# Optimization experiments

Measured on AMD Instinct MI355X. Metric: run time of the kernel, lower is better.

Reference implementation:

```python
import jax, jax.numpy as jnp
import numpy as np

N, E, G = 30000, 240000, 128
D_IN, D_H, D_OUT, HEADS = 128, 128, 16, 4
EPS_BN = 1e-5


def setup_inputs() -> dict:
    key = jax.random.key(0)
    ks = jax.random.split(key, 24)
    s = 0.1
    inp = {
        "x": jax.random.normal(ks[0], (N, D_IN), jnp.float32),
        "edge_index": jax.random.randint(ks[1], (2, E), 0, N, jnp.int32),
        "batch": jnp.sort(jax.random.randint(ks[2], (N,), 0, G, jnp.int32)),
        # stacked per-layer params (3 GAT blocks, identical shapes since D_IN==D_H)
        "W": jax.random.normal(ks[3], (3, D_H, HEADS * D_H), jnp.float32) * s,
        "att_src": jax.random.normal(ks[4], (3, HEADS, D_H), jnp.float32) * s,
        "att_dst": jax.random.normal(ks[5], (3, HEADS, D_H), jnp.float32) * s,
        "conv_b": jnp.zeros((3, D_H), jnp.float32),
        "gamma": jnp.ones((3, D_H), jnp.float32),
        "beta": jnp.zeros((3, D_H), jnp.float32),
        "sk_Win": jax.random.normal(ks[6], (3, D_H, D_H), jnp.float32) * s,
        "sk_bin": jnp.zeros((3, D_H), jnp.float32),
        "sk_Wout": jax.random.normal(ks[7], (3, D_H, D_H), jnp.float32) * s,
        "sk_bout": jnp.zeros((3, D_H), jnp.float32),
        "fc1_W": jax.random.normal(ks[8], (D_H, D_H), jnp.float32) * s,
        "fc1_b": jnp.zeros((D_H,), jnp.float32),
        "fc3_W": jax.random.normal(ks[9], (D_H, D_OUT), jnp.float32) * s,
        "fc3_b": jnp.zeros((D_OUT,), jnp.float32),
    }
    return inp


def _gat_conv(x, src, dst, W, a_src, a_dst, b):
    # PyG GATConv, heads=4, concat=False (mean over heads), leaky_relu 0.2
    h = (x @ W).reshape(N, HEADS, D_H)                      # [N,H,C]
    al_s = jnp.einsum('nhc,hc->nh', h, a_src)               # [N,H]
    al_d = jnp.einsum('nhc,hc->nh', h, a_dst)
    e = jax.nn.leaky_relu(al_s[src] + al_d[dst], 0.2)       # [Etot,H]
    m = jax.ops.segment_max(e, dst, num_segments=N)
    m = jnp.where(jnp.isfinite(m), m, 0.0)
    ex = jnp.exp(e - m[dst])
    z = jax.ops.segment_sum(ex, dst, num_segments=N)
    alpha = ex / (z[dst] + 1e-16)                           # [Etot,H]
    msg = h[src] * alpha[:, :, None]                        # [Etot,H,C]
    out = jax.ops.segment_sum(msg, dst, num_segments=N)     # [N,H,C]
    return out.mean(axis=1) + b


def _batch_norm(h, gamma, beta):
    mu = h.mean(axis=0)
    var = h.var(axis=0)
    return gamma * (h - mu) * jax.lax.rsqrt(var + EPS_BN) + beta


def _gated_skip(in_x, out_x, Win, bin_, Wout, bout):
    gate = jax.nn.sigmoid(in_x @ Win + bin_ + out_x @ Wout + bout)
    return gate * out_x + (1.0 - gate) * in_x


def reference(x, edge_index, batch, W, att_src, att_dst, conv_b, gamma, beta,
              sk_Win, sk_bin, sk_Wout, sk_bout, fc1_W, fc1_b, fc3_W, fc3_b):
    # add self loops (PyG GATConv default)
    loops = jnp.arange(N, dtype=edge_index.dtype)
    src = jnp.concatenate([edge_index[0], loops])
    dst = jnp.concatenate([edge_index[1], loops])

    h = x
    for l in range(3):
        idn = h
        h = _gat_conv(h, src, dst, W[l], att_src[l], att_dst[l], conv_b[l])
        h = _batch_norm(h, gamma[l], beta[l])
        h = _gated_skip(idn, h, sk_Win[l], sk_bin[l], sk_Wout[l], sk_bout[l])
        h = jax.nn.relu(h)

    # global mean pool over graphs
    cnt = jax.ops.segment_sum(jnp.ones((N,), h.dtype), batch, num_segments=G)
    hg = jax.ops.segment_sum(h, batch, num_segments=G) / jnp.maximum(cnt, 1.0)[:, None]
    hg = jax.nn.relu(hg @ fc1_W + fc1_b)
    return hg @ fc3_W + fc3_b
```

## Files before the change

kernel.cpp:

```cpp
#include <hip/hip_runtime.h>
#include <hip/hip_bf16.h>

#define N_NODES 30000
#define N_EDGES 240000
#define ETOT    (N_EDGES + N_NODES)
#define NGRAPH  128
#define NBLK    118
#define NWAVES  4096

typedef __attribute__((ext_vector_type(8))) short bf16x8;
typedef __attribute__((ext_vector_type(4))) short bf16x4;
typedef __attribute__((ext_vector_type(4))) float f32x4;

__device__ __forceinline__ unsigned short f2bf(float f) {
    unsigned u = __float_as_uint(f);
    u += 0x7fff + ((u >> 16) & 1);
    return (unsigned short)(u >> 16);
}
__device__ __forceinline__ float bf2f(unsigned short h) {
    return __uint_as_float(((unsigned)h) << 16);
}

__global__ __launch_bounds__(256) void prep_kernel(const float* __restrict__ W,
                                                   const float* __restrict__ Win,
                                                   const float* __restrict__ Wout,
                                                   const float* __restrict__ x,
                                                   const int* __restrict__ batch,
                                                   short* __restrict__ wt_hi,
                                                   short* __restrict__ wint_hi,
                                                   short* __restrict__ woutt_hi,
                                                   short* __restrict__ xb,
                                                   int* __restrict__ gstart,
                                                   int* __restrict__ deg,
                                                   float* __restrict__ bnsum) {
    int i = blockIdx.x * 256 + threadIdx.x;
    if (i < 196608) {
        int l = i >> 16, r = i & 65535;
        int n = r >> 7, k = r & 127;
        wt_hi[i] = (short)f2bf(W[(size_t)l * 65536 + k * 512 + n]);
    } else if (i < 245760) {
        int j = i - 196608;
        int l = j >> 14, r = j & 16383;
        int n = r >> 7, k = r & 127;
        wint_hi[j] = (short)f2bf(Win[(size_t)l * 16384 + k * 128 + n]);
    } else if (i < 294912) {
        int j = i - 245760;
        int l = j >> 14, r = j & 16383;
        int n = r >> 7, k = r & 127;
        woutt_hi[j] = (short)f2bf(Wout[(size_t)l * 16384 + k * 128 + n]);
    } else if (i < 774912) {
        int j = i - 294912;
        const float4* p = (const float4*)x + (size_t)j * 2;
        float4 v0 = p[0], v1 = p[1];
        bf16x8 hv;
        hv[0] = (short)f2bf(v0.x); hv[1] = (short)f2bf(v0.y);
        hv[2] = (short)f2bf(v0.z); hv[3] = (short)f2bf(v0.w);
        hv[4] = (short)f2bf(v1.x); hv[5] = (short)f2bf(v1.y);
        hv[6] = (short)f2bf(v1.z); hv[7] = (short)f2bf(v1.w);
        *(bf16x8*)(xb + (size_t)j * 8) = hv;
    } else if (i < 775041) {
        int t = i - 774912;
        int lo = 0, hi = N_NODES;
        while (lo < hi) { int mid = (lo + hi) >> 1; if (batch[mid] < t) lo = mid + 1; else hi = mid; }
        gstart[t] = lo;
    } else if (i < 805041) {
        deg[i - 775041] = 0;
    } else if (i < 805809) {
        bnsum[i - 805041] = 0.f;
    }
}

__global__ __launch_bounds__(256) void gemm_conv(const short* __restrict__ Ab,
                                                 const short* __restrict__ Bth,
                                                 const float* __restrict__ att_s,
                                                 const float* __restrict__ att_d,
                                                 unsigned short* __restrict__ hfullb,
                                                 float* __restrict__ als,
                                                 float* __restrict__ ald) {
    __shared__ short As_h[64 * 136];
    __shared__ float red_s[2][64], red_d[2][64];
    const int bm = blockIdx.x * 64;
    const int hd = blockIdx.y;
    const int bn = hd * 128;
    const int t  = threadIdx.x;
#pragma unroll
    for (int i = 0; i < 4; i++) {
        int idx8 = t + i * 256;
        int row = idx8 >> 4, c8 = (idx8 & 15) << 3;
        bf16x8 vh = {};
        if (bm + row < N_NODES)
            vh = *(const bf16x8*)(Ab + (size_t)(bm + row) * 128 + c8);
        *(bf16x8*)(As_h + row * 136 + c8) = vh;
    }
    __syncthreads();

    const int w = t >> 6, lane = t & 63;
    const int wr = w >> 1, wc = w & 1;
    const int lr = lane & 15, lg = lane >> 4;
    f32x4 acc[2][4] = {};
    const size_t bofs0 = (size_t)(bn + wc * 64 + lr) * 128 + lg * 8;
#pragma unroll
    for (int kk = 0; kk < 4; kk++) {
        bf16x8 ah[2], bh[4];
#pragma unroll
        for (int ni = 0; ni < 4; ni++) {
            size_t o = bofs0 + (size_t)ni * 16 * 128 + kk * 32;
            bh[ni] = *(const bf16x8*)(Bth + o);
        }
        int ko = kk * 32 + lg * 8;
#pragma unroll
        for (int mi = 0; mi < 2; mi++) {
            int r = wr * 32 + mi * 16 + lr;
            ah[mi] = *(const bf16x8*)(As_h + r * 136 + ko);
        }
#pragma unroll
        for (int mi = 0; mi < 2; mi++)
#pragma unroll
            for (int ni = 0; ni < 4; ni++)
                acc[mi][ni] = __builtin_amdgcn_mfma_f32_16x16x32_bf16(ah[mi], bh[ni], acc[mi][ni], 0, 0, 0);
    }
    float as_c[4], ad_c[4];
#pragma unroll
    for (int ni = 0; ni < 4; ni++) {
        int cc = wc * 64 + ni * 16 + lr;
        as_c[ni] = att_s[hd * 128 + cc];
        ad_c[ni] = att_d[hd * 128 + cc];
    }
#pragma unroll
    for (int mi = 0; mi < 2; mi++) {
#pragma unroll
        for (int r = 0; r < 4; r++) {
            float ps = 0.f, pd = 0.f;
#pragma unroll
            for (int ni = 0; ni < 4; ni++) {
                ps = fmaf(acc[mi][ni][r], as_c[ni], ps);
                pd = fmaf(acc[mi][ni][r], ad_c[ni], pd);
            }
#pragma unroll
            for (int off = 1; off < 16; off <<= 1) {
                ps += __shfl_xor(ps, off);
                pd += __shfl_xor(pd, off);
            }
            if (lr == 0) {
                int row = wr * 32 + mi * 16 + lg * 4 + r;
                red_s[wc][row] = ps;
                red_d[wc][row] = pd;
            }
        }
    }
    __syncthreads();
#pragma unroll
    for (int mi = 0; mi < 2; mi++)
#pragma unroll
        for (int ni = 0; ni < 4; ni++) {
            int nl = wc * 64 + ni * 16 + lr;
#pragma unroll
            for (int r = 0; r < 4; r++) {
                int row = wr * 32 + mi * 16 + lg * 4 + r;
                As_h[row * 136 + nl] = (short)f2bf(acc[mi][ni][r]);
            }
        }
    if (t < 64) {
        int m = bm + t;
        if (m < N_NODES) als[m * 4 + hd] = red_s[0][t] + red_s[1][t];
    } else if (t < 128) {
        int tt = t - 64;
        int m = bm + tt;
        if (m < N_NODES) ald[m * 4 + hd] = red_d[0][tt] + red_d[1][tt];
    }
    __syncthreads();
#pragma unroll
    for (int i2 = 0; i2 < 4; i2++) {
        int idx8 = t + i2 * 256;
        int row = idx8 >> 4, c8 = (idx8 & 15) << 3;
        int m = bm + row;
        if (m < N_NODES)
            *(bf16x8*)(hfullb + (size_t)m * 512 + bn + c8) = *(const bf16x8*)(As_h + row * 136 + c8);
    }
}

__global__ __launch_bounds__(256) void skip_conv(const short* __restrict__ hinb,
                                                 const float* __restrict__ g,
                                                 const float* __restrict__ bnsum,
                                                 const float* __restrict__ gamma,
                                                 const float* __restrict__ beta,
                                                 const short* __restrict__ w1h,
                                                 const short* __restrict__ w2h,
                                                 const float* __restrict__ bin,
                                                 const float* __restrict__ bout,
                                                 const short* __restrict__ wtn,
                                                 const float* __restrict__ att_s,
                                                 const float* __restrict__ att_d,
                                                 short* __restrict__ houtb,
                                                 unsigned short* __restrict__ hfullb,
                                                 float* __restrict__ als,
                                                 float* __restrict__ ald) {
    __shared__ short A1h[64 * 136], A2h[64 * 136];
    __shared__ float bnp_s[256];
    __shared__ float redS[4][64], redD[4][64];
    const int bm = blockIdx.x * 64;
    const int t  = threadIdx.x;
    if (t < 128) {
        float inv = 1.f / (float)N_NODES;
        float mu  = bnsum[t] * inv;
        float var = bnsum[128 + t] * inv - mu * mu;
        float rs  = rsqrtf(var + 1e-5f);
        float sc  = gamma[t] * rs;
        bnp_s[t]       = sc;
        bnp_s[128 + t] = beta[t] - mu * sc;
    }
    __syncthreads();
#pragma unroll
    for (int i = 0; i < 4; i++) {
        int idx8 = t + i * 256;
        int row = idx8 >> 4, c8 = (idx8 & 15) << 3;
        bf16x8 vh = {};
        if (bm + row < N_NODES)
            vh = *(const bf16x8*)(hinb + (size_t)(bm + row) * 128 + c8);
        *(bf16x8*)(A1h + row * 136 + c8) = vh;
    }
#pragma unroll
    for (int i = 0; i < 8; i++) {
        int idx4 = t + i * 256;
        int row = idx4 >> 5, c4 = (idx4 & 31) << 2;
        float4 v2 = make_float4(0.f, 0.f, 0.f, 0.f);
        if (bm + row < N_NODES) {
            float4 gv = *(const float4*)(g + (size_t)(bm + row) * 128 + c4);
            v2.x = fmaf(bnp_s[c4 + 0], gv.x, bnp_s[128 + c4 + 0]);
            v2.y = fmaf(bnp_s[c4 + 1], gv.y, bnp_s[128 + c4 + 1]);
            v2.z = fmaf(bnp_s[c4 + 2], gv.z, bnp_s[128 + c4 + 2]);
            v2.w = fmaf(bnp_s[c4 + 3], gv.w, bnp_s[128 + c4 + 3]);
        }
        *(bf16x4*)(A2h + row * 136 + c4) = (bf16x4){(short)f2bf(v2.x), (short)f2bf(v2.y),
                                                    (short)f2bf(v2.z), (short)f2bf(v2.w)};
    }
    __syncthreads();

    const int w = t >> 6, lane = t & 63;
    const int wr = w >> 1, wc = w & 1;
    const int lr = lane & 15, lg = lane >> 4;

    {
        f32x4 acc[2][4] = {};
        const size_t bo = (size_t)(wc * 64 + lr) * 128 + lg * 8;
#pragma unroll
        for (int kk = 0; kk < 4; kk++) {
            bf16x8 a1[2], a2[2], b1[4], b2[4];
#pragma unroll
            for (int ni = 0; ni < 4; ni++) {
                size_t o = bo + (size_t)ni * 2048 + kk * 32;
                b1[ni] = *(const bf16x8*)(w1h + o);
                b2[ni] = *(const bf16x8*)(w2h + o);
            }
            int ko = kk * 32 + lg * 8;
#pragma unroll
            for (int mi = 0; mi < 2; mi++) {
                int r = wr * 32 + mi * 16 + lr;
                a1[mi] = *(const bf16x8*)(A1h + r * 136 + ko);
                a2[mi] = *(const bf16x8*)(A2h + r * 136 + ko);
            }
#pragma unroll
            for (int mi = 0; mi < 2; mi++)
#pragma unroll
                for (int ni = 0; ni < 4; ni++) {
                    acc[mi][ni] = __builtin_amdgcn_mfma_f32_16x16x32_bf16(a1[mi], b1[ni], acc[mi][ni], 0, 0, 0);
                    acc[mi][ni] = __builtin_amdgcn_mfma_f32_16x16x32_bf16(a2[mi], b2[ni], acc[mi][ni], 0, 0, 0);
                }
        }
#pragma unroll
        for (int mi = 0; mi < 2; mi++)
#pragma unroll
            for (int ni = 0; ni < 4; ni++) {
                int n = wc * 64 + ni * 16 + lr;
                float bsum = bin[n] + bout[n];
                float sc = bnp_s[n], shb = bnp_s[128 + n];
#pragma unroll
                for (int r = 0; r < 4; r++) {
                    int lrow = wr * 32 + mi * 16 + lg * 4 + r;
                    int m = bm + lrow;
                    float gv = (m < N_NODES) ? g[(size_t)m * 128 + n] : 0.f;
                    float hbnv = fmaf(sc, gv, shb);
                    float hv   = bf2f((unsigned short)A1h[lrow * 136 + n]);
                    float gt   = 1.f / (1.f + __expf(-(acc[mi][ni][r] + bsum)));
                    acc[mi][ni][r] = fmaxf(gt * hbnv + (1.f - gt) * hv, 0.f);
                }
            }
        __syncthreads();
#pragma unroll
        for (int mi = 0; mi < 2; mi++)
#pragma unroll
            for (int ni = 0; ni < 4; ni++) {
                int n = wc * 64 + ni * 16 + lr;
#pragma unroll
                for (int r = 0; r < 4; r++) {
                    int lrow = wr * 32 + mi * 16 + lg * 4 + r;
                    A1h[lrow * 136 + n] = (short)f2bf(acc[mi][ni][r]);
                }
            }
        __syncthreads();
#pragma unroll
        for (int i2 = 0; i2 < 4; i2++) {
            int idx8 = t + i2 * 256;
            int row = idx8 >> 4, c8 = (idx8 & 15) << 3;
            int m = bm + row;
            if (m < N_NODES)
                *(bf16x8*)(houtb + (size_t)m * 128 + c8) = *(const bf16x8*)(A1h + row * 136 + c8);
        }
    }

    f32x4 c2[4][8] = {};
    const int hd = w;
    const size_t bo2 = (size_t)(hd * 128 + lr) * 128 + lg * 8;
#pragma unroll
    for (int kk = 0; kk < 4; kk++) {
        bf16x8 ah2[4], bh2[8];
#pragma unroll
        for (int ni = 0; ni < 8; ni++)
            bh2[ni] = *(const bf16x8*)(wtn + bo2 + (size_t)ni * 2048 + kk * 32);
        int ko = kk * 32 + lg * 8;
#pragma unroll
        for (int mi = 0; mi < 4; mi++)
            ah2[mi] = *(const bf16x8*)(A1h + (mi * 16 + lr) * 136 + ko);
#pragma unroll
        for (int mi = 0; mi < 4; mi++)
#pragma unroll
            for (int ni = 0; ni < 8; ni++)
                c2[mi][ni] = __builtin_amdgcn_mfma_f32_16x16x32_bf16(ah2[mi], bh2[ni], c2[mi][ni], 0, 0, 0);
    }
    {
        float asc[8], adc[8];
#pragma unroll
        for (int ni = 0; ni < 8; ni++) {
            int cc = ni * 16 + lr;
            asc[ni] = att_s[hd * 128 + cc];
            adc[ni] = att_d[hd * 128 + cc];
        }
#pragma unroll
        for (int mi = 0; mi < 4; mi++)
#pragma unroll
            for (int r = 0; r < 4; r++) {
                float ps = 0.f, pd = 0.f;
#pragma unroll
                for (int ni = 0; ni < 8; ni++) {
                    ps = fmaf(c2[mi][ni][r], asc[ni], ps);
                    pd = fmaf(c2[mi][ni][r], adc[ni], pd);
                }
#pragma unroll
                for (int off = 1; off < 16; off <<= 1) {
                    ps += __shfl_xor(ps, off);
                    pd += __shfl_xor(pd, off);
                }
                if (lr == 0) {
                    int row = mi * 16 + lg * 4 + r;
                    redS[hd][row] = ps;
                    redD[hd][row] = pd;
                }
            }
    }
    __syncthreads();
    if (w < 2) {
        short* dst = (w == 0) ? A1h : A2h;
#pragma unroll
        for (int mi = 0; mi < 4; mi++)
#pragma unroll
            for (int ni = 0; ni < 8; ni++)
#pragma unroll
                for (int r = 0; r < 4; r++)
                    dst[(mi * 16 + lg * 4 + r) * 136 + ni * 16 + lr] = (short)f2bf(c2[mi][ni][r]);
    }
    {
        int hd2 = t >> 6, row = t & 63;
        int m = bm + row;
        if (m < N_NODES) {
            als[m * 4 + hd2] = redS[hd2][row];
            ald[m * 4 + hd2] = redD[hd2][row];
        }
    }
    __syncthreads();
#pragma unroll
    for (int it = 0; it < 8; it++) {
        int idx = t + it * 256;
        int row = idx >> 5, c8 = (idx & 31) << 3;
        int m = bm + row;
        if (m < N_NODES) {
            const short* src = (c8 < 128) ? A1h : A2h;
            *(bf16x8*)(hfullb + (size_t)m * 512 + c8) = *(const bf16x8*)(src + row * 136 + (c8 & 127));
        }
    }
    __syncthreads();
    if (w >= 2) {
        short* dst = (w == 2) ? A1h : A2h;
#pragma unroll
        for (int mi = 0; mi < 4; mi++)
#pragma unroll
            for (int ni = 0; ni < 8; ni++)
#pragma unroll
                for (int r = 0; r < 4; r++)
                    dst[(mi * 16 + lg * 4 + r) * 136 + ni * 16 + lr] = (short)f2bf(c2[mi][ni][r]);
    }
    __syncthreads();
#pragma unroll
    for (int it = 0; it < 8; it++) {
        int idx = t + it * 256;
        int row = idx >> 5, c8 = (idx & 31) << 3;
        int m = bm + row;
        if (m < N_NODES) {
            const short* src = (c8 < 128) ? A1h : A2h;
            *(bf16x8*)(hfullb + (size_t)m * 512 + 256 + c8) = *(const bf16x8*)(src + row * 136 + (c8 & 127));
        }
    }
}

__global__ __launch_bounds__(256) void skip_gate(const short* __restrict__ hinb,
                                                 const float* __restrict__ g,
                                                 const float* __restrict__ bnsum,
                                                 const float* __restrict__ gamma,
                                                 const float* __restrict__ beta,
                                                 const short* __restrict__ w1h,
                                                 const short* __restrict__ w2h,
                                                 const float* __restrict__ bin, const float* __restrict__ bout,
                                                 short* __restrict__ houtb) {
    __shared__ short A1h[64 * 136], A2h[64 * 136], A2l[64 * 136];
    __shared__ float bnp_s[256];
    const int bm = blockIdx.x * 64;
    const int bn = blockIdx.y * 64;
    const int t  = threadIdx.x;
    if (t < 128) {
        float inv = 1.f / (float)N_NODES;
        float mu  = bnsum[t] * inv;
        float var = bnsum[128 + t] * inv - mu * mu;
        float rs  = rsqrtf(var + 1e-5f);
        float sc  = gamma[t] * rs;
        bnp_s[t]       = sc;
        bnp_s[128 + t] = beta[t] - mu * sc;
    }
    __syncthreads();
#pragma unroll
    for (int i = 0; i < 4; i++) {
        int idx8 = t + i * 256;
        int row = idx8 >> 4, c8 = (idx8 & 15) << 3;
        bf16x8 vh = {};
        if (bm + row < N_NODES)
            vh = *(const bf16x8*)(hinb + (size_t)(bm + row) * 128 + c8);
        *(bf16x8*)(A1h + row * 136 + c8) = vh;
    }
#pragma unroll
    for (int i = 0; i < 8; i++) {
        int idx4 = t + i * 256;
        int row = idx4 >> 5, c4 = (idx4 & 31) << 2;
        float4 v2 = make_float4(0.f, 0.f, 0.f, 0.f);
        if (bm + row < N_NODES) {
            float4 gv = *(const float4*)(g + (size_t)(bm + row) * 128 + c4);
            v2.x = fmaf(bnp_s[c4 + 0], gv.x, bnp_s[128 + c4 + 0]);
            v2.y = fmaf(bnp_s[c4 + 1], gv.y, bnp_s[128 + c4 + 1]);
            v2.z = fmaf(bnp_s[c4 + 2], gv.z, bnp_s[128 + c4 + 2]);
            v2.w = fmaf(bnp_s[c4 + 3], gv.w, bnp_s[128 + c4 + 3]);
        }
        unsigned short b0 = f2bf(v2.x), b1 = f2bf(v2.y), b2 = f2bf(v2.z), b3 = f2bf(v2.w);
        *(bf16x4*)(A2h + row * 136 + c4) = (bf16x4){(short)b0, (short)b1, (short)b2, (short)b3};
        *(bf16x4*)(A2l + row * 136 + c4) = (bf16x4){(short)f2bf(v2.x - bf2f(b0)), (short)f2bf(v2.y - bf2f(b1)),
                                                    (short)f2bf(v2.z - bf2f(b2)), (short)f2bf(v2.w - bf2f(b3))};
    }
    __syncthreads();

    const int w = t >> 6, lane = t & 63;
    const int wr = w >> 1, wc = w & 1;
    const int lr = lane & 15, lg = lane >> 4;
    f32x4 acc[2][2] = {};
    const size_t bofs0 = (size_t)(bn + wc * 32 + lr) * 128 + lg * 8;
#pragma unroll
    for (int kk = 0; kk < 4; kk++) {
        bf16x8 a1f[2], a2f[2], b1h[2], b2h[2];
#pragma unroll
        for (int ni = 0; ni < 2; ni++) {
            size_t o = bofs0 + (size_t)ni * 16 * 128 + kk * 32;
            b1h[ni] = *(const bf16x8*)(w1h + o);
            b2h[ni] = *(const bf16x8*)(w2h + o);
        }
        int ko = kk * 32 + lg * 8;
#pragma unroll
        for (int mi = 0; mi < 2; mi++) {
            int r = wr * 32 + mi * 16 + lr;
            a1f[mi] = *(const bf16x8*)(A1h + r * 136 + ko);
            a2f[mi] = *(const bf16x8*)(A2h + r * 136 + ko);
        }
#pragma unroll
        for (int mi = 0; mi < 2; mi++)
#pragma unroll
            for (int ni = 0; ni < 2; ni++) {
                acc[mi][ni] = __builtin_amdgcn_mfma_f32_16x16x32_bf16(a1f[mi], b1h[ni], acc[mi][ni], 0, 0, 0);
                acc[mi][ni] = __builtin_amdgcn_mfma_f32_16x16x32_bf16(a2f[mi], b2h[ni], acc[mi][ni], 0, 0, 0);
            }
    }
#pragma unroll
    for (int mi = 0; mi < 2; mi++) {
#pragma unroll
        for (int ni = 0; ni < 2; ni++) {
            int n = bn + wc * 32 + ni * 16 + lr;
            float bsum = bin[n] + bout[n];
#pragma unroll
            for (int r = 0; r < 4; r++) {
                int lrow = wr * 32 + mi * 16 + lg * 4 + r;
                float hbnv = bf2f((unsigned short)A2h[lrow * 136 + n]) + bf2f((unsigned short)A2l[lrow * 136 + n]);
                float hv   = bf2f((unsigned short)A1h[lrow * 136 + n]);
                float gt   = 1.f / (1.f + __expf(-(acc[mi][ni][r] + bsum)));
                acc[mi][ni][r] = fmaxf(gt * hbnv + (1.f - gt) * hv, 0.f);
            }
        }
    }
    __syncthreads();
#pragma unroll
    for (int mi = 0; mi < 2; mi++)
#pragma unroll
        for (int ni = 0; ni < 2; ni++) {
            int n = bn + wc * 32 + ni * 16 + lr;
#pragma unroll
            for (int r = 0; r < 4; r++) {
                int lrow = wr * 32 + mi * 16 + lg * 4 + r;
                A1h[lrow * 136 + n] = (short)f2bf(acc[mi][ni][r]);
            }
        }
    __syncthreads();
#pragma unroll
    for (int i2 = 0; i2 < 2; i2++) {
        int idx8 = t + i2 * 256;
        int row = idx8 >> 3, c8 = (idx8 & 7) << 3;
        int m = bm + row;
        if (m < N_NODES)
            *(bf16x8*)(houtb + (size_t)m * 128 + bn + c8) = *(const bf16x8*)(A1h + row * 136 + bn + c8);
    }
}

__global__ __launch_bounds__(256) void deg_kernel(const int* __restrict__ ei1,
                                                  int* __restrict__ deg) {
    int e = blockIdx.x * 256 + threadIdx.x;
    if (e >= ETOT) return;
    int d = (e < N_EDGES) ? ei1[e] : (e - N_EDGES);
    atomicAdd(&deg[d], 1);
}

__global__ __launch_bounds__(256) void scan1(const int* __restrict__ deg,
                                             int* __restrict__ tmp,
                                             int* __restrict__ blksum) {
    int i = blockIdx.x * 256 + threadIdx.x;
    int v = (i < N_NODES) ? deg[i] : 0;
    __shared__ int sh[256];
    sh[threadIdx.x] = v;
    __syncthreads();
    int acc = v;
    for (int off = 1; off < 256; off <<= 1) {
        int u = (threadIdx.x >= off) ? sh[threadIdx.x - off] : 0;
        __syncthreads();
        acc += u;
        sh[threadIdx.x] = acc;
        __syncthreads();
    }
    if (i < N_NODES) tmp[i] = acc - v;
    if (threadIdx.x == 255) blksum[blockIdx.x] = acc;
}

__global__ void scan2(const int* __restrict__ blksum, int* __restrict__ blkoff) {
    int t = threadIdx.x;
    int v = (t < NBLK) ? blksum[t] : 0;
    __shared__ int sh[128];
    sh[t] = v;
    __syncthreads();
    int acc = v;
    for (int off = 1; off < 128; off <<= 1) {
        int u = (t >= off) ? sh[t - off] : 0;
        __syncthreads();
        acc += u;
        sh[t] = acc;
        __syncthreads();
    }
    if (t < NBLK) blkoff[t] = acc - v;
}

__global__ __launch_bounds__(256) void scan3(const int* __restrict__ tmp,
                                             const int* __restrict__ blkoff,
                                             int* __restrict__ rowptr,
                                             int* __restrict__ wofs) {
    int i = blockIdx.x * 256 + threadIdx.x;
    if (i == 0) rowptr[N_NODES] = ETOT;
    if (i < N_NODES) {
        int r = tmp[i] + blkoff[blockIdx.x];
        rowptr[i] = r;
        wofs[i]   = r;
    }
}

__global__ __launch_bounds__(256) void wpart_kernel(const int* __restrict__ rowptr,
                                                    int* __restrict__ wstart) {
    int wid = blockIdx.x * 256 + threadIdx.x;
    if (wid > NWAVES) return;
    if (wid == NWAVES) { wstart[NWAVES] = N_NODES; return; }
    int target = (int)(((long)wid * ETOT) / NWAVES);
    int lo = 0, hi = N_NODES;
    while (lo < hi) { int mid = (lo + hi) >> 1; if (rowptr[mid] < target) lo = mid + 1; else hi = mid; }
    wstart[wid] = lo;
}

__global__ __launch_bounds__(256) void scatter_kernel(const int* __restrict__ ei0,
                                                      const int* __restrict__ ei1,
                                                      int* __restrict__ wofs,
                                                      int* __restrict__ csr_src) {
    int e = blockIdx.x * 256 + threadIdx.x;
    if (e >= ETOT) return;
    int s = (e < N_EDGES) ? ei0[e] : (e - N_EDGES);
    int d = (e < N_EDGES) ? ei1[e] : (e - N_EDGES);
    int pos = atomicAdd(&wofs[d], 1);
    csr_src[pos] = s;
}

__global__ __launch_bounds__(256) void gat_gather(const int* __restrict__ rowptr,
                                                  const int* __restrict__ wstart,
                                                  const int* __restrict__ csr_src,
                                                  const float* __restrict__ al_s,
                                                  const float* __restrict__ al_d,
                                                  const unsigned short* __restrict__ hfullb,
                                                  const float* __restrict__ conv_b,
                                                  float* __restrict__ g,
                                                  float* __restrict__ bnsum,
                                                  float* __restrict__ bnsum2) {
    const int lane = threadIdx.x & 63;
    const int wib  = threadIdx.x >> 6;
    const int gwid = blockIdx.x * 4 + wib;
    const int h    = lane >> 4;
    const int sub  = lane & 15;
    float s1[8] = {}, s2[8] = {};

    const int n0 = wstart[gwid], n1 = wstart[gwid + 1];
    for (int n = n0; n < n1; n++) {
        const int e0 = rowptr[n], e1 = rowptr[n + 1];
        const float ald_h = al_d[n * 4 + h];

        float acc[8] = {};
        float zs = 0.f;
        int i = e0;
        for (; i + 3 < e1; i += 4) {
            int sA = csr_src[i], sB = csr_src[i + 1], sC = csr_src[i + 2], sD = csr_src[i + 3];
            bf16x8 ha = *(const bf16x8*)(hfullb + (size_t)sA * 512 + lane * 8);
            bf16x8 hb = *(const bf16x8*)(hfullb + (size_t)sB * 512 + lane * 8);
            bf16x8 hc = *(const bf16x8*)(hfullb + (size_t)sC * 512 + lane * 8);
            bf16x8 hd = *(const bf16x8*)(hfullb + (size_t)sD * 512 + lane * 8);
            float vA = al_s[sA * 4 + h] + ald_h; vA = (vA > 0.f) ? vA : 0.2f * vA;
            float vB = al_s[sB * 4 + h] + ald_h; vB = (vB > 0.f) ? vB : 0.2f * vB;
            float vC = al_s[sC * 4 + h] + ald_h; vC = (vC > 0.f) ? vC : 0.2f * vC;
            float vD = al_s[sD * 4 + h] + ald_h; vD = (vD > 0.f) ? vD : 0.2f * vD;
            float exA = __expf(vA), exB = __expf(vB), exC = __expf(vC), exD = __expf(vD);
            zs += (exA + exB) + (exC + exD);
#pragma unroll
            for (int j = 0; j < 8; j++) {
                float a = fmaf(exA, bf2f((unsigned short)ha[j]), acc[j]);
                a = fmaf(exB, bf2f((unsigned short)hb[j]), a);
                a = fmaf(exC, bf2f((unsigned short)hc[j]), a);
                acc[j] = fmaf(exD, bf2f((unsigned short)hd[j]), a);
            }
        }
        for (; i < e1; i++) {
            int sA = csr_src[i];
            bf16x8 ha = *(const bf16x8*)(hfullb + (size_t)sA * 512 + lane * 8);
            float vA = al_s[sA * 4 + h] + ald_h; vA = (vA > 0.f) ? vA : 0.2f * vA;
            float exA = __expf(vA);
            zs += exA;
#pragma unroll
            for (int j = 0; j < 8; j++)
                acc[j] = fmaf(exA, bf2f((unsigned short)ha[j]), acc[j]);
        }

        float inv = 0.25f / (zs + 1e-16f);
#pragma unroll
        for (int j = 0; j < 8; j++) {
            float a = acc[j] * inv;
            a += __shfl_xor(a, 16);
            a += __shfl_xor(a, 32);
            acc[j] = a;
        }
        if (lane < 16) {
            float o[8];
#pragma unroll
            for (int j = 0; j < 8; j++) {
                float tv = acc[j] + conv_b[sub * 8 + j];
                o[j] = tv;
                s1[j] += tv;
                s2[j] = fmaf(tv, tv, s2[j]);
            }
            float* gp = g + (size_t)n * 128 + sub * 8;
            *(float4*)gp       = make_float4(o[0], o[1], o[2], o[3]);
            *(float4*)(gp + 4) = make_float4(o[4], o[5], o[6], o[7]);
        }
    }

    __shared__ float redA[4][128], redB[4][128];
    if (lane < 16) {
#pragma unroll
        for (int j = 0; j < 8; j++) {
            redA[wib][sub * 8 + j] = s1[j];
            redB[wib][sub * 8 + j] = s2[j];
        }
    }
    __syncthreads();
    int t = threadIdx.x;
    if (t < 128) {
        atomicAdd(&bnsum[t], redA[0][t] + redA[1][t] + redA[2][t] + redA[3][t]);
    } else {
        int c = t - 128;
        atomicAdd(&bnsum2[c], redB[0][c] + redB[1][c] + redB[2][c] + redB[3][c]);
    }
}

__global__ __launch_bounds__(1024) void pool_head(const short* __restrict__ hb,
                                                  const int* __restrict__ gstart,
                                                  const float* __restrict__ fc1W,
                                                  const float* __restrict__ fc1b,
                                                  const float* __restrict__ fc3W,
                                                  const float* __restrict__ fc3b,
                                                  float* __restrict__ out) {
    int gid = blockIdx.x, t = threadIdx.x;
    int lo = gstart[gid], hi = gstart[gid + 1];
    int c = t & 127, q = t >> 7;
    float s = 0.f;
    for (int n = lo + q; n < hi; n += 8)
        s += bf2f((unsigned short)hb[(size_t)n * 128 + c]);
    __shared__ float sh[1024];
    __shared__ float hg[128], a1[128];
    sh[t] = s;
    __syncthreads();
    if (t < 128) {
        float cc = fmaxf((float)(hi - lo), 1.f);
        float tot = 0.f;
#pragma unroll
        for (int q2 = 0; q2 < 8; q2++) tot += sh[q2 * 128 + t];
        hg[t] = tot / cc;
    }
    __syncthreads();
    {
        int oc = t & 127, ch = t >> 7;
        float v = 0.f;
#pragma unroll
        for (int k = 0; k < 16; k++) {
            int c2 = ch * 16 + k;
            v = fmaf(hg[c2], fc1W[c2 * 128 + oc], v);
        }
        sh[t] = v;
    }
    __syncthreads();
    if (t < 128) {
        float v = fc1b[t];
#pragma unroll
        for (int q2 = 0; q2 < 8; q2++) v += sh[q2 * 128 + t];
        a1[t] = fmaxf(v, 0.f);
    }
    __syncthreads();
    if (t < 16) {
        float o = fc3b[t];
        for (int j = 0; j < 128; j++) o = fmaf(a1[j], fc3W[j * 16 + t], o);
        out[gid * 16 + t] = o;
    }
}

extern "C" void kernel_launch(void* const* d_in, const int* in_sizes, int n_in,
                              void* d_out, int out_size, void* d_ws, size_t ws_size,
                              hipStream_t stream) {
    const float* x       = (const float*)d_in[0];
    const int*   ei      = (const int*)d_in[1];
    const int*   batch   = (const int*)d_in[2];
    const float* W       = (const float*)d_in[3];
    const float* att_src = (const float*)d_in[4];
    const float* att_dst = (const float*)d_in[5];
    const float* conv_b  = (const float*)d_in[6];
    const float* gamma   = (const float*)d_in[7];
    const float* beta    = (const float*)d_in[8];
    const float* sk_Win  = (const float*)d_in[9];
    const float* sk_bin  = (const float*)d_in[10];
    const float* sk_Wout = (const float*)d_in[11];
    const float* sk_bout = (const float*)d_in[12];
    const float* fc1_W   = (const float*)d_in[13];
    const float* fc1_b   = (const float*)d_in[14];
    const float* fc3_W   = (const float*)d_in[15];
    const float* fc3_b   = (const float*)d_in[16];
    float* out = (float*)d_out;
    const int* ei0 = ei;
    const int* ei1 = ei + N_EDGES;

    float* ws = (float*)d_ws;
    size_t o = 0;
    unsigned short* hfullb = (unsigned short*)(ws + o); o += (size_t)N_NODES * 256;
    float* gbuf   = ws + o; o += (size_t)N_NODES * 128;
    short* hbA    = (short*)(ws + o); o += (size_t)N_NODES * 64;
    short* hbB    = (short*)(ws + o); o += (size_t)N_NODES * 64;
    float* als    = ws + o; o += N_NODES * 4;
    float* ald    = ws + o; o += N_NODES * 4;
    float* bnsum  = ws + o; o += 768;
    short* wt_hi   = (short*)(ws + o); o += 98304;
    short* wint_hi = (short*)(ws + o); o += 24576;
    short* woutt_hi = (short*)(ws + o); o += 24576;
    int* gstart   = (int*)(ws + o); o += 132;
    int* deg      = (int*)(ws + o); o += N_NODES;
    int* rowptr   = (int*)(ws + o); o += N_NODES + 4;
    int* wofs     = (int*)(ws + o); o += N_NODES;
    int* scantmp  = (int*)(ws + o); o += N_NODES;
    int* blksum   = (int*)(ws + o); o += NBLK + 2;
    int* blkoff   = (int*)(ws + o); o += NBLK + 2;
    int* wstart   = (int*)(ws + o); o += NWAVES + 2;
    int* csr_src  = (int*)(ws + o); o += ETOT;

    prep_kernel<<<3148, 256, 0, stream>>>(W, sk_Win, sk_Wout, x, batch,
                                          wt_hi, wint_hi, woutt_hi, hbA, gstart, deg, bnsum);

    deg_kernel<<<(ETOT + 255) / 256, 256, 0, stream>>>(ei1, deg);
    scan1<<<NBLK, 256, 0, stream>>>(deg, scantmp, blksum);
    scan2<<<1, 128, 0, stream>>>(blksum, blkoff);
    scan3<<<NBLK, 256, 0, stream>>>(scantmp, blkoff, rowptr, wofs);
    wpart_kernel<<<17, 256, 0, stream>>>(rowptr, wstart);
    scatter_kernel<<<(ETOT + 255) / 256, 256, 0, stream>>>(ei0, ei1, wofs, csr_src);

    gemm_conv<<<dim3(469, 4), 256, 0, stream>>>(hbA, wt_hi, att_src, att_dst, hfullb, als, ald);
    gat_gather<<<1024, 256, 0, stream>>>(rowptr, wstart, csr_src, als, ald, hfullb,
                                         conv_b, gbuf, bnsum, bnsum + 128);
    skip_conv<<<469, 256, 0, stream>>>(hbA, gbuf, bnsum, gamma, beta,
                                       wint_hi, woutt_hi, sk_bin, sk_bout,
                                       wt_hi + 65536, att_src + 512, att_dst + 512,
                                       hbB, hfullb, als, ald);
    gat_gather<<<1024, 256, 0, stream>>>(rowptr, wstart, csr_src, als, ald, hfullb,
                                         conv_b + 128, gbuf, bnsum + 256, bnsum + 384);
    skip_conv<<<469, 256, 0, stream>>>(hbB, gbuf, bnsum + 256, gamma + 128, beta + 128,
                                       wint_hi + 16384, woutt_hi + 16384, sk_bin + 128, sk_bout + 128,
                                       wt_hi + 131072, att_src + 1024, att_dst + 1024,
                                       hbA, hfullb, als, ald);
    gat_gather<<<1024, 256, 0, stream>>>(rowptr, wstart, csr_src, als, ald, hfullb,
                                         conv_b + 256, gbuf, bnsum + 512, bnsum + 640);
    skip_gate<<<dim3(469, 2), 256, 0, stream>>>(hbA, gbuf, bnsum + 512, gamma + 256, beta + 256,
                                                wint_hi + 32768, woutt_hi + 32768,
                                                sk_bin + 256, sk_bout + 256, hbB);

    pool_head<<<NGRAPH, 1024, 0, stream>>>(hbB, gstart, fc1_W, fc1_b, fc3_W, fc3_b, out);
}
```

Baseline: 390.0 us.

## Fuse global mean pooling into final skip-gate epilogue via atomics

The final gated-skip kernel no longer writes the bf16 node features. Instead it sums each tile's rows per graph id in registers, reduces them across lanes with shuffles, and atomically adds the sums into a per-graph pooled buffer that the prep kernel zeroes. The pool_head kernel now only divides by the node counts and runs the small MLP with 128 threads. This drops one node-feature write and re-read and the bf16 rounding before pooling, at the cost of float atomics and a nondeterministic summation order. The gather output stores also become nontemporal.

After: 392.7 us. No clear change (+0.7%).

```diff
diff --git a/kernel.cpp b/kernel.cpp
--- a/kernel.cpp
+++ b/kernel.cpp
@@ -32,7 +32,8 @@
                                                    short* __restrict__ xb,
                                                    int* __restrict__ gstart,
                                                    int* __restrict__ deg,
-                                                   float* __restrict__ bnsum) {
+                                                   float* __restrict__ bnsum,
+                                                   float* __restrict__ pooled) {
     int i = blockIdx.x * 256 + threadIdx.x;
     if (i < 196608) {
         int l = i >> 16, r = i & 65535;
@@ -67,6 +68,8 @@
         deg[i - 775041] = 0;
     } else if (i < 805809) {
         bnsum[i - 805041] = 0.f;
+    } else if (i < 822193) {
+        pooled[i - 805809] = 0.f;
     }
 }
 
@@ -419,7 +422,8 @@
                                                  const short* __restrict__ w1h,
                                                  const short* __restrict__ w2h,
                                                  const float* __restrict__ bin, const float* __restrict__ bout,
-                                                 short* __restrict__ houtb) {
+                                                 const int* __restrict__ batch,
+                                                 float* __restrict__ pooled) {
     __shared__ short A1h[64 * 136], A2h[64 * 136], A2l[64 * 136];
     __shared__ float bnp_s[256];
     const int bm = blockIdx.x * 64;
@@ -508,26 +512,32 @@
             }
         }
     }
-    __syncthreads();
+    int gidv[2][4];
 #pragma unroll
     for (int mi = 0; mi < 2; mi++)
 #pragma unroll
+        for (int r = 0; r < 4; r++) {
+            int m = bm + wr * 32 + mi * 16 + lg * 4 + r;
+            gidv[mi][r] = (m < N_NODES) ? batch[m] : -1;
+        }
+    int g0 = batch[bm];
+    int glast = batch[(bm + 63 < N_NODES) ? (bm + 63) : (N_NODES - 1)];
+    for (int gg = g0; gg <= glast; gg++) {
+#pragma unroll
         for (int ni = 0; ni < 2; ni++) {
-            int n = bn + wc * 32 + ni * 16 + lr;
-#pragma unroll
-            for (int r = 0; r < 4; r++) {
-                int lrow = wr * 32 + mi * 16 + lg * 4 + r;
-                A1h[lrow * 136 + n] = (short)f2bf(acc[mi][ni][r]);
-            }
-        }
-    __syncthreads();
-#pragma unroll
-    for (int i2 = 0; i2 < 2; i2++) {
-        int idx8 = t + i2 * 256;
-        int row = idx8 >> 3, c8 = (idx8 & 7) << 3;
-        int m = bm + row;
-        if (m < N_NODES)
-            *(bf16x8*)(houtb + (size_t)m * 128 + bn + c8) = *(const bf16x8*)(A1h + row * 136 + bn + c8);
+            float s = 0.f;
+#pragma unroll
+            for (int mi = 0; mi < 2; mi++)
+#pragma unroll
+                for (int r = 0; r < 4; r++)
+                    if (gidv[mi][r] == gg) s += acc[mi][ni][r];
+            s += __shfl_xor(s, 16);
+            s += __shfl_xor(s, 32);
+            if (lg == 0) {
+                int n = bn + wc * 32 + ni * 16 + lr;
+                atomicAdd(&pooled[gg * 128 + n], s);
+            }
+        }
     }
 }
 
@@ -686,8 +696,10 @@
                 s2[j] = fmaf(tv, tv, s2[j]);
             }
             float* gp = g + (size_t)n * 128 + sub * 8;
-            *(float4*)gp       = make_float4(o[0], o[1], o[2], o[3]);
-            *(float4*)(gp + 4) = make_float4(o[4], o[5], o[6], o[7]);
+            f32x4 w0 = {o[0], o[1], o[2], o[3]};
+            f32x4 w1 = {o[4], o[5], o[6], o[7]};
+            __builtin_nontemporal_store(w0, (f32x4*)gp);
+            __builtin_nontemporal_store(w1, (f32x4*)(gp + 4));
         }
     }
 
@@ -709,48 +721,21 @@
     }
 }
 
-__global__ __launch_bounds__(1024) void pool_head(const short* __restrict__ hb,
-                                                  const int* __restrict__ gstart,
-                                                  const float* __restrict__ fc1W,
-                                                  const float* __restrict__ fc1b,
-                                                  const float* __restrict__ fc3W,
-                                                  const float* __restrict__ fc3b,
-                                                  float* __restrict__ out) {
+__global__ __launch_bounds__(128) void pool_head(const float* __restrict__ pooled,
+                                                 const int* __restrict__ gstart,
+                                                 const float* __restrict__ fc1W,
+                                                 const float* __restrict__ fc1b,
+                                                 const float* __restrict__ fc3W,
+                                                 const float* __restrict__ fc3b,
+                                                 float* __restrict__ out) {
     int gid = blockIdx.x, t = threadIdx.x;
-    int lo = gstart[gid], hi = gstart[gid + 1];
-    int c = t & 127, q = t >> 7;
-    float s = 0.f;
-    for (int n = lo + q; n < hi; n += 8)
-        s += bf2f((unsigned short)hb[(size_t)n * 128 + c]);
-    __shared__ float sh[1024];
     __shared__ float hg[128], a1[128];
-    sh[t] = s;
-    __syncthreads();
-    if (t < 128) {
-        float cc = fmaxf((float)(hi - lo), 1.f);
-        float tot = 0.f;
-#pragma unroll
-        for (int q2 = 0; q2 < 8; q2++) tot += sh[q2 * 128 + t];
-        hg[t] = tot / cc;
-    }
-    __syncthreads();
-    {
-        int oc = t & 127, ch = t >> 7;
-        float v = 0.f;
-#pragma unroll
-        for (int k = 0; k < 16; k++) {
-            int c2 = ch * 16 + k;
-            v = fmaf(hg[c2], fc1W[c2 * 128 + oc], v);
-        }
-        sh[t] = v;
-    }
-    __syncthreads();
-    if (t < 128) {
-        float v = fc1b[t];
-#pragma unroll
-        for (int q2 = 0; q2 < 8; q2++) v += sh[q2 * 128 + t];
-        a1[t] = fmaxf(v, 0.f);
-    }
+    float cc = fmaxf((float)(gstart[gid + 1] - gstart[gid]), 1.f);
+    hg[t] = pooled[gid * 128 + t] / cc;
+    __syncthreads();
+    float v = fc1b[t];
+    for (int c2 = 0; c2 < 128; c2++) v = fmaf(hg[c2], fc1W[c2 * 128 + t], v);
+    a1[t] = fmaxf(v, 0.f);
     __syncthreads();
     if (t < 16) {
         float o = fc3b[t];
@@ -792,6 +777,7 @@
     float* als    = ws + o; o += N_NODES * 4;
     float* ald    = ws + o; o += N_NODES * 4;
     float* bnsum  = ws + o; o += 768;
+    float* pooled = ws + o; o += NGRAPH * 128;
     short* wt_hi   = (short*)(ws + o); o += 98304;
     short* wint_hi = (short*)(ws + o); o += 24576;
     short* woutt_hi = (short*)(ws + o); o += 24576;
@@ -805,8 +791,8 @@
     int* wstart   = (int*)(ws + o); o += NWAVES + 2;
     int* csr_src  = (int*)(ws + o); o += ETOT;
 
-    prep_kernel<<<3148, 256, 0, stream>>>(W, sk_Win, sk_Wout, x, batch,
-                                          wt_hi, wint_hi, woutt_hi, hbA, gstart, deg, bnsum);
+    prep_kernel<<<3212, 256, 0, stream>>>(W, sk_Win, sk_Wout, x, batch,
+                                          wt_hi, wint_hi, woutt_hi, hbA, gstart, deg, bnsum, pooled);
 
     deg_kernel<<<(ETOT + 255) / 256, 256, 0, stream>>>(ei1, deg);
     scan1<<<NBLK, 256, 0, stream>>>(deg, scantmp, blksum);
@@ -832,7 +818,7 @@
                                          conv_b + 256, gbuf, bnsum + 512, bnsum + 640);
     skip_gate<<<dim3(469, 2), 256, 0, stream>>>(hbA, gbuf, bnsum + 512, gamma + 256, beta + 256,
                                                 wint_hi + 32768, woutt_hi + 32768,
-                                                sk_bin + 256, sk_bout + 256, hbB);
-
-    pool_head<<<NGRAPH, 1024, 0, stream>>>(hbB, gstart, fc1_W, fc1_b, fc3_W, fc3_b, out);
-}
+                                                sk_bin + 256, sk_bout + 256, batch, pooled);
+
+    pool_head<<<NGRAPH, 128, 0, stream>>>(pooled, gstart, fc1_W, fc1_b, fc3_W, fc3_b, out);
+}
```
